# Kernel optimization log

Hardware: AMD Instinct MI355X
Metric: run time of the kernel (lower is better)

## Reference

```python
import jax, jax.numpy as jnp
import numpy as np

N = 50000      # nodes
E = 800000     # edges (avg degree 16)
D_IN, D_H, D_OUT = 128, 256, 128


def setup_inputs() -> dict:
    key = jax.random.key(0)
    ks = jax.random.split(key, 12)
    x = jax.random.normal(ks[0], (N, D_IN), jnp.float32)
    src = jax.random.randint(ks[1], (E,), 0, N)
    dst = jax.random.randint(ks[2], (E,), 0, N)

    def lin(k, din, dout):
        return (jax.random.normal(k, (din, dout), jnp.float32) / np.sqrt(din)).astype(jnp.float32)

    dims = [(D_IN, D_H), (D_H, D_H), (D_H, D_OUT)]
    params = {}
    ki = 3
    for i, (di, do) in enumerate(dims):
        params[f"W_self{i}"] = lin(ks[ki], di, do); ki += 1
        params[f"W_neigh{i}"] = lin(ks[ki], di, do); ki += 1
        params[f"b{i}"] = jnp.zeros((do,), jnp.float32)
    return {"x": x, "src": src, "dst": dst, **params}


def _mean_agg(h, src, dst):
    # gather src features along edges, segment-mean into dst nodes
    msg = jnp.take(h, src, axis=0)                              # [E, D]
    s = jax.ops.segment_sum(msg, dst, num_segments=N)           # [N, D]
    deg = jax.ops.segment_sum(jnp.ones((dst.shape[0], 1), h.dtype), dst, num_segments=N)
    return s / jnp.maximum(deg, 1.0)                            # zero-degree -> 0, as in DGL


def reference(x, src, dst,
              W_self0, W_neigh0, b0,
              W_self1, W_neigh1, b1,
              W_self2, W_neigh2, b2):
    Ws = [(W_self0, W_neigh0, b0), (W_self1, W_neigh1, b1), (W_self2, W_neigh2, b2)]
    h = x
    for i, (Ws_i, Wn_i, b_i) in enumerate(Ws):
        neigh = _mean_agg(h, src, dst)
        h = h @ Ws_i + neigh @ Wn_i + b_i                       # SAGEConv('mean')
        if i < len(Ws) - 1:
            h = jax.nn.relu(h)                                  # activation between layers
    return h
```

## Files before the change

### kernel.cpp

```cpp
#include <hip/hip_runtime.h>

#define NN 50000
#define NE 800000
#define NCHK 200
#define CHKE 4000
#define NBUK 196
#define BCAP 5120
#define NOFF (NBUK * NCHK)
#define NSB  ((NOFF + 255) / 256)

typedef __attribute__((ext_vector_type(8))) short short8;
typedef __attribute__((ext_vector_type(4))) float f32x4;
typedef unsigned int u32;
typedef unsigned short u16;

__device__ __forceinline__ float bf2f(short u) {
    union { unsigned int i; float f; } c;
    c.i = ((unsigned int)(unsigned short)u) << 16;
    return c.f;
}
__device__ __forceinline__ short f2bf(float f) {
    union { float f; unsigned int i; } c; c.f = f;
    unsigned int u = c.i;
    unsigned int r = (u + 0x7FFFu + ((u >> 16) & 1u)) >> 16;
    return (short)r;
}


__global__ void cvt_f32_bf16_kernel(const float* __restrict__ in, short* __restrict__ out, int n) {
    int gid = blockIdx.x * 256 + threadIdx.x;
    if (gid < n) out[gid] = f2bf(in[gid]);
}

__global__ void wcvt_all_kernel(const float* __restrict__ Ws0, const float* __restrict__ Wn0,
                                const float* __restrict__ Ws1, const float* __restrict__ Wn1,
                                const float* __restrict__ Ws2, const float* __restrict__ Wn2,
                                short* __restrict__ wts) {
    int gid = blockIdx.x * 256 + threadIdx.x;
    const float* W; int K, Dout, base, loc;
    if (gid < 65536)       { K = 128; Dout = 256; base = (gid < 32768)  ? 0 : 32768;
                             W = (gid < 32768)  ? Ws0 : Wn0; loc = gid & 32767; }
    else if (gid < 196608) { K = 256; Dout = 256; base = (gid < 131072) ? 65536 : 131072;
                             W = (gid < 131072) ? Ws1 : Wn1; loc = (gid - 65536) & 65535; }
    else                   { K = 256; Dout = 128; base = (gid < 229376) ? 196608 : 229376;
                             W = (gid < 229376) ? Ws2 : Wn2; loc = (gid - 196608) & 32767; }
    int k = loc / Dout, d = loc - k * Dout;
    int kt = k >> 6, kl = k & 63;
    wts[base + kt * Dout * 64 + d * 64 + (kl ^ ((d & 7) << 3))] = f2bf(W[(long)k * Dout + d]);
}

__global__ __launch_bounds__(256) void bucket_hist_kernel(const int* __restrict__ dst,
                                                          int* __restrict__ chist) {
    __shared__ int lh[NBUK];
    int b = blockIdx.x, t = threadIdx.x;
    for (int i = t; i < NBUK; i += 256) lh[i] = 0;
    __syncthreads();
    int base = b * CHKE;
    for (int i = t; i < CHKE; i += 256) atomicAdd(&lh[dst[base + i] >> 8], 1);
    __syncthreads();
    for (int i = t; i < NBUK; i += 256) chist[i * NCHK + b] = lh[i];
}

__global__ __launch_bounds__(256) void off_blocksum_kernel(const int* __restrict__ in,
                                                           int* __restrict__ bsum) {
    __shared__ int sm[256];
    int t = threadIdx.x;
    int idx = blockIdx.x * 256 + t;
    sm[t] = (idx < NOFF) ? in[idx] : 0;
    __syncthreads();
    for (int off = 128; off > 0; off >>= 1) {
        if (t < off) sm[t] += sm[t + off];
        __syncthreads();
    }
    if (t == 0) bsum[blockIdx.x] = sm[0];
}

__global__ __launch_bounds__(256) void off_scanb_kernel(const int* __restrict__ bsum,
                                                        int* __restrict__ bpre) {
    __shared__ int sm[256];
    int t = threadIdx.x;
    sm[t] = (t < NSB) ? bsum[t] : 0;
    __syncthreads();
    for (int o = 1; o < 256; o <<= 1) {
        int v = sm[t];
        int a = (t >= o) ? sm[t - o] : 0;
        __syncthreads();
        sm[t] = v + a;
        __syncthreads();
    }
    if (t < NSB) bpre[t] = (t == 0) ? 0 : sm[t - 1];
}

__global__ __launch_bounds__(256) void off_scatter_kernel(const int* __restrict__ in,
                                                          const int* __restrict__ bpre,
                                                          int* __restrict__ off) {
    __shared__ int sm[256];
    int t = threadIdx.x;
    int idx = blockIdx.x * 256 + t;
    int val = (idx < NOFF) ? in[idx] : 0;
    sm[t] = val;
    __syncthreads();
    for (int o = 1; o < 256; o <<= 1) {
        int v = sm[t];
        int a = (t >= o) ? sm[t - o] : 0;
        __syncthreads();
        sm[t] = v + a;
        __syncthreads();
    }
    if (idx < NOFF) off[idx] = bpre[blockIdx.x] + sm[t] - val;
}

__global__ __launch_bounds__(256) void bucket_scatter_kernel(const int* __restrict__ src,
                                                             const int* __restrict__ dst,
                                                             const int* __restrict__ off,
                                                             u32* __restrict__ ebuf) {
    __shared__ int lcur[NBUK];
    int b = blockIdx.x, t = threadIdx.x;
    for (int i = t; i < NBUK; i += 256) lcur[i] = off[i * NCHK + b];
    __syncthreads();
    int base = b * CHKE;
    for (int i = t; i < CHKE; i += 256) {
        int d = dst[base + i], s = src[base + i];
        int slot = atomicAdd(&lcur[d >> 8], 1);
        ebuf[slot] = ((u32)(d & 255) << 16) | (u32)s;
    }
}

__global__ __launch_bounds__(256) void bucket_sort_kernel(const u32* __restrict__ ebuf,
                                                          const int* __restrict__ off,
                                                          u16* __restrict__ srcs16,
                                                          int* __restrict__ row_start,
                                                          int* __restrict__ cnt) {
    __shared__ u32 earr[BCAP];
    __shared__ u16 s16[BCAP];
    __shared__ int lhist[256], lpre[256], lcur[256];
    int k = blockIdx.x, t = threadIdx.x;
    int base = off[k * NCHK];
    int end  = (k < NBUK - 1) ? off[(k + 1) * NCHK] : NE;
    int nE = end - base;
    lhist[t] = 0;
    __syncthreads();
    for (int i = t; i < nE; i += 256) {
        u32 e = ebuf[base + i];
        earr[i] = e;
        atomicAdd(&lhist[e >> 16], 1);
    }
    __syncthreads();
    int v = lhist[t];
    lpre[t] = v;
    __syncthreads();
    for (int o = 1; o < 256; o <<= 1) {
        int x = lpre[t];
        int a = (t >= o) ? lpre[t - o] : 0;
        __syncthreads();
        lpre[t] = x + a;
        __syncthreads();
    }
    int excl = lpre[t] - v;
    int node = k * 256 + t;
    if (node < NN) { row_start[node] = base + excl; cnt[node] = v; }
    lcur[t] = excl;
    __syncthreads();
    for (int i = t; i < nE; i += 256) {
        u32 e = earr[i];
        int pos = atomicAdd(&lcur[e >> 16], 1);
        s16[pos] = (u16)(e & 0xFFFFu);
    }
    __syncthreads();
    for (int i = t; i < nE; i += 256) srcs16[base + i] = s16[i];
}


template<int D>
__global__ __launch_bounds__(256) void gather_mean2_kernel(
    const short* __restrict__ h, const u16* __restrict__ srcs,
    const int* __restrict__ row_start, const int* __restrict__ cnt,
    short* __restrict__ nb)
{
    constexpr int CPR = D / 8;
    constexpr int EPL = 64 / CPR;
    const int wave = threadIdx.x >> 6;
    const int lane = threadIdx.x & 63;
    const int v = blockIdx.x * 4 + wave;
    if (v >= NN) return;
    const int c  = cnt[v];
    const int rs = row_start[v];
    const int slot = lane / CPR;
    const int cg   = lane & (CPR - 1);
    float acc[8];
    #pragma unroll
    for (int j = 0; j < 8; ++j) acc[j] = 0.f;
    const short8* hp = (const short8*)h;
    int i = slot;
    for (; i + 3 * EPL < c; i += 4 * EPL) {
        int s0 = srcs[rs + i];
        int s1 = srcs[rs + i + EPL];
        int s2 = srcs[rs + i + 2 * EPL];
        int s3 = srcs[rs + i + 3 * EPL];
        short8 v0 = hp[(size_t)s0 * CPR + cg];
        short8 v1 = hp[(size_t)s1 * CPR + cg];
        short8 v2 = hp[(size_t)s2 * CPR + cg];
        short8 v3 = hp[(size_t)s3 * CPR + cg];
        #pragma unroll
        for (int j = 0; j < 8; ++j)
            acc[j] += (bf2f(v0[j]) + bf2f(v1[j])) + (bf2f(v2[j]) + bf2f(v3[j]));
    }
    for (; i < c; i += EPL) {
        int s0 = srcs[rs + i];
        short8 v0 = hp[(size_t)s0 * CPR + cg];
        #pragma unroll
        for (int j = 0; j < 8; ++j) acc[j] += bf2f(v0[j]);
    }
    #pragma unroll
    for (int j = 0; j < 8; ++j) {
        if (EPL == 4) acc[j] += __shfl_xor(acc[j], 16);
        acc[j] += __shfl_xor(acc[j], 32);
    }
    if (slot == 0) {
        float inv = (c > 0) ? (1.0f / (float)c) : 0.0f;
        short8 outv;
        #pragma unroll
        for (int j = 0; j < 8; ++j) outv[j] = f2bf(acc[j] * inv);
        ((short8*)nb)[(size_t)v * CPR + cg] = outv;
    }
}

template<int NOUT, int KK, int PHASES, bool RELU, bool OUT_F32, bool ADDIN, bool BIAS>
__global__ __launch_bounds__(512, 2) void gemm_sage3_kernel(
    const short* __restrict__ Aself, const short* __restrict__ Aneigh,
    const short* __restrict__ Bself, const short* __restrict__ Bneigh,
    const float* __restrict__ bias, void* __restrict__ outp, int M,
    const short* __restrict__ addin)
{
    constexpr int WN = NOUT / 64;
    constexpr int WM = 8 / WN;
    constexpr int MR = 128 / (WM * 16);
    constexpr int NR = 4;
    constexpr int KT = KK / 64;
    constexpr int NT = PHASES * KT;
    constexpr int WC = NOUT / 64;

    __shared__ short ldsA[2][128 * 64];
    __shared__ short ldsW[2][NOUT * 64];

    const int tid  = threadIdx.x;
    const int wave = tid >> 6;
    const int lane = tid & 63;
    const int wm = wave / WN;
    const int wn = wave % WN;
    const int l15 = lane & 15;
    const int kg  = lane >> 4;
    const int bm  = blockIdx.x * 128;

    f32x4 acc[MR][NR];
    #pragma unroll
    for (int a = 0; a < MR; ++a)
        #pragma unroll
        for (int b = 0; b < NR; ++b)
            acc[a][b] = (f32x4){0.f, 0.f, 0.f, 0.f};

    const int srow = tid >> 3;
    const int scol = ((tid & 7) << 3) ^ ((srow & 7) << 3);

    auto stageA = [&](int buf, int t) {
        int ph = t / KT, kt = t - ph * KT;
        const short* A = ph ? Aneigh : Aself;
        #pragma unroll
        for (int c = 0; c < 2; ++c) {
            const short* gp = A + (size_t)(bm + c * 64 + srow) * KK + kt * 64 + scol;
            __builtin_amdgcn_global_load_lds(
                (const __attribute__((address_space(1))) u32*)gp,
                (__attribute__((address_space(3))) u32*)(&ldsA[buf][c * 4096 + (wave << 9)]),
                16, 0, 0);
        }
    };
    auto stageW = [&](int buf, int t) {
        int ph = t / KT, kt = t - ph * KT;
        const short* Wm = (ph ? Bneigh : Bself) + (size_t)kt * NOUT * 64 + tid * 8;
        #pragma unroll
        for (int c = 0; c < WC; ++c) {
            __builtin_amdgcn_global_load_lds(
                (const __attribute__((address_space(1))) u32*)(Wm + c * 4096),
                (__attribute__((address_space(3))) u32*)(&ldsW[buf][c * 4096 + (wave << 9)]),
                16, 0, 0);
        }
    };

    stageA(0, 0);
    stageW(0, 0);
    __syncthreads();

    for (int t = 0; t < NT; ++t) {
        const int cur = t & 1;
        if (t + 1 < NT) { stageA(cur ^ 1, t + 1); stageW(cur ^ 1, t + 1); }

        #pragma unroll
        for (int ks = 0; ks < 2; ++ks) {
            short8 areg[MR], wreg[NR];
            #pragma unroll
            for (int mr = 0; mr < MR; ++mr) {
                int r = wm * (MR * 16) + mr * 16 + l15;
                areg[mr] = *(const short8*)(&ldsA[cur][r * 64 + ((ks * 32 + kg * 8) ^ ((r & 7) << 3))]);
            }
            #pragma unroll
            for (int nr = 0; nr < NR; ++nr) {
                int cl = wn * 64 + nr * 16 + l15;
                wreg[nr] = *(const short8*)(&ldsW[cur][cl * 64 + ((ks * 32 + kg * 8) ^ ((cl & 7) << 3))]);
            }
            #pragma unroll
            for (int mr = 0; mr < MR; ++mr)
                #pragma unroll
                for (int nr = 0; nr < NR; ++nr)
                    acc[mr][nr] = __builtin_amdgcn_mfma_f32_16x16x32_bf16(
                        areg[mr], wreg[nr], acc[mr][nr], 0, 0, 0);
        }
        __syncthreads();
    }

    #pragma unroll
    for (int mr = 0; mr < MR; ++mr) {
        int rowb = bm + wm * (MR * 16) + mr * 16 + kg * 4;
        #pragma unroll
        for (int nr = 0; nr < NR; ++nr) {
            int col = wn * 64 + nr * 16 + l15;
            float bv = BIAS ? bias[col] : 0.f;
            #pragma unroll
            for (int r = 0; r < 4; ++r) {
                int row = rowb + r;
                if (row < M) {
                    float vv = acc[mr][nr][r] + bv;
                    if (ADDIN) vv += bf2f(addin[(size_t)row * NOUT + col]);
                    if (RELU) vv = fmaxf(vv, 0.f);
                    if (OUT_F32) ((float*)outp)[(size_t)row * NOUT + col] = vv;
                    else         ((short*)outp)[(size_t)row * NOUT + col] = f2bf(vv);
                }
            }
        }
    }
}


extern "C" void kernel_launch(void* const* d_in, const int* in_sizes, int n_in,
                              void* d_out, int out_size, void* d_ws, size_t ws_size,
                              hipStream_t stream) {
    const float* x    = (const float*)d_in[0];
    const int*   srcp = (const int*)d_in[1];
    const int*   dstp = (const int*)d_in[2];
    const float* Ws0  = (const float*)d_in[3];
    const float* Wn0  = (const float*)d_in[4];
    const float* b0   = (const float*)d_in[5];
    const float* Ws1  = (const float*)d_in[6];
    const float* Wn1  = (const float*)d_in[7];
    const float* b1   = (const float*)d_in[8];
    const float* Ws2  = (const float*)d_in[9];
    const float* Wn2  = (const float*)d_in[10];
    const float* b2   = (const float*)d_in[11];

    char* base = (char*)d_ws;
    size_t off_b = 0;
    auto alloc = [&](size_t bytes) -> void* {
        void* p = base + off_b;
        off_b += (bytes + 255) & ~(size_t)255;
        return p;
    };

    int*   cnt       = (int*)alloc((size_t)NN * 4);
    int*   row_start = (int*)alloc((size_t)NN * 4);
    int*   chist     = (int*)alloc((size_t)NOFF * 4);
    int*   offb      = (int*)alloc((size_t)NOFF * 4);
    int*   bsum      = (int*)alloc((size_t)NSB * 4);
    int*   bpre      = (int*)alloc((size_t)NSB * 4);
    u32*   ebuf      = (u32*)alloc((size_t)NE * 4);
    u16*   srcs16    = (u16*)alloc((size_t)NE * 2);
    short* hA        = (short*)alloc((size_t)NN * 256 * 2);
    short* hB        = (short*)alloc((size_t)NN * 256 * 2);
    short* nb        = (short*)alloc((size_t)NN * 256 * 2);
    short* wts       = (short*)alloc((size_t)262144 * 2 + 65536);
    short* Wt0s = wts;
    short* Wt0n = Wt0s + 32768;
    short* Wt1s = Wt0n + 32768;
    short* Wt1n = Wt1s + 65536;
    short* Wt2s = Wt1n + 65536;
    short* Wt2n = Wt2s + 32768;

    bucket_hist_kernel<<<NCHK, 256, 0, stream>>>(dstp, chist);
    off_blocksum_kernel<<<NSB, 256, 0, stream>>>(chist, bsum);
    off_scanb_kernel<<<1, 256, 0, stream>>>(bsum, bpre);
    off_scatter_kernel<<<NSB, 256, 0, stream>>>(chist, bpre, offb);
    bucket_scatter_kernel<<<NCHK, 256, 0, stream>>>(srcp, dstp, offb, ebuf);
    bucket_sort_kernel<<<NBUK, 256, 0, stream>>>(ebuf, offb, srcs16, row_start, cnt);

    wcvt_all_kernel<<<1024, 256, 0, stream>>>(Ws0, Wn0, Ws1, Wn1, Ws2, Wn2, wts);

    cvt_f32_bf16_kernel<<<(NN * 128 + 255) / 256, 256, 0, stream>>>(x, hA, NN * 128);

    const int mblocks = (NN + 127) / 128;
    const int gblocks = (NN + 3) / 4;

    gather_mean2_kernel<128><<<gblocks, 256, 0, stream>>>(hA, srcs16, row_start, cnt, nb);
    gemm_sage3_kernel<256, 128, 2, true, false, false, true><<<mblocks, 512, 0, stream>>>(
        hA, nb, Wt0s, Wt0n, b0, hB, NN, nullptr);

    gather_mean2_kernel<256><<<gblocks, 256, 0, stream>>>(hB, srcs16, row_start, cnt, nb);
    gemm_sage3_kernel<256, 256, 2, true, false, false, true><<<mblocks, 512, 0, stream>>>(
        hB, nb, Wt1s, Wt1n, b1, hA, NN, nullptr);

    gemm_sage3_kernel<128, 256, 1, false, false, false, false><<<mblocks, 512, 0, stream>>>(
        hA, hA, Wt2n, Wt2n, nullptr, hB, NN, nullptr);
    gather_mean2_kernel<128><<<gblocks, 256, 0, stream>>>(hB, srcs16, row_start, cnt, nb);
    gemm_sage3_kernel<128, 256, 1, false, true, true, true><<<mblocks, 512, 0, stream>>>(
        hA, hA, Wt2s, Wt2s, b2, d_out, NN, nb);
}
```

Baseline: 243.2 us.

## Load GEMM weights straight into registers in MFMA fragment order, drop LDS staging

The weight conversion kernel now writes each weight matrix in the exact per-lane MFMA fragment order. The GEMM kernel then loads a whole phase of weight fragments from global memory straight into registers, instead of double-buffering weight tiles through LDS. This removes the weight LDS buffers, the weight staging traffic and the LDS reads of weights from the inner loop. In exchange, each lane holds KT*2*NR short8 weight registers per phase alongside the accumulators, which risks register spills under the 512-thread, 2-blocks launch bound.

```diff
diff --git a/kernel.cpp b/kernel.cpp
--- a/kernel.cpp
+++ b/kernel.cpp
@@ -45,8 +45,10 @@
     else                   { K = 256; Dout = 128; base = (gid < 229376) ? 196608 : 229376;
                              W = (gid < 229376) ? Ws2 : Wn2; loc = (gid - 196608) & 32767; }
     int k = loc / Dout, d = loc - k * Dout;
-    int kt = k >> 6, kl = k & 63;
-    wts[base + kt * Dout * 64 + d * 64 + (kl ^ ((d & 7) << 3))] = f2bf(W[(long)k * Dout + d]);
+    int kt = k >> 6, ks = (k >> 5) & 1, kg = (k >> 3) & 3, j = k & 7;
+    int cgp = d >> 4, l = d & 15;
+    int off = ((((kt * 2 + ks) * (Dout >> 4) + cgp) * 4 + kg) * 16 + l) * 8 + j;
+    wts[base + off] = f2bf(W[(long)k * Dout + d]);
 }
 
 __global__ __launch_bounds__(256) void bucket_hist_kernel(const int* __restrict__ dst,
@@ -226,7 +228,7 @@
 }
 
 template<int NOUT, int KK, int PHASES, bool RELU, bool OUT_F32, bool ADDIN, bool BIAS>
-__global__ __launch_bounds__(512, 2) void gemm_sage3_kernel(
+__global__ __launch_bounds__(512, 2) void gemm_sage4_kernel(
     const short* __restrict__ Aself, const short* __restrict__ Aneigh,
     const short* __restrict__ Bself, const short* __restrict__ Bneigh,
     const float* __restrict__ bias, void* __restrict__ outp, int M,
@@ -238,10 +240,9 @@
     constexpr int NR = 4;
     constexpr int KT = KK / 64;
     constexpr int NT = PHASES * KT;
-    constexpr int WC = NOUT / 64;
+    constexpr int CG = NOUT / 16;
 
     __shared__ short ldsA[2][128 * 64];
-    __shared__ short ldsW[2][NOUT * 64];
 
     const int tid  = threadIdx.x;
     const int wave = tid >> 6;
@@ -274,47 +275,46 @@
                 16, 0, 0);
         }
     };
-    auto stageW = [&](int buf, int t) {
-        int ph = t / KT, kt = t - ph * KT;
-        const short* Wm = (ph ? Bneigh : Bself) + (size_t)kt * NOUT * 64 + tid * 8;
-        #pragma unroll
-        for (int c = 0; c < WC; ++c) {
-            __builtin_amdgcn_global_load_lds(
-                (const __attribute__((address_space(1))) u32*)(Wm + c * 4096),
-                (__attribute__((address_space(3))) u32*)(&ldsW[buf][c * 4096 + (wave << 9)]),
-                16, 0, 0);
-        }
-    };
 
     stageA(0, 0);
-    stageW(0, 0);
-    __syncthreads();
-
-    for (int t = 0; t < NT; ++t) {
-        const int cur = t & 1;
-        if (t + 1 < NT) { stageA(cur ^ 1, t + 1); stageW(cur ^ 1, t + 1); }
-
-        #pragma unroll
-        for (int ks = 0; ks < 2; ++ks) {
-            short8 areg[MR], wreg[NR];
+    __syncthreads();
+
+    #pragma unroll
+    for (int ph = 0; ph < PHASES; ++ph) {
+        const short* __restrict__ Wb = ph ? Bneigh : Bself;
+        short8 wreg[KT][2][NR];
+        #pragma unroll
+        for (int kt = 0; kt < KT; ++kt)
             #pragma unroll
-            for (int mr = 0; mr < MR; ++mr) {
-                int r = wm * (MR * 16) + mr * 16 + l15;
-                areg[mr] = *(const short8*)(&ldsA[cur][r * 64 + ((ks * 32 + kg * 8) ^ ((r & 7) << 3))]);
-            }
-            #pragma unroll
-            for (int nr = 0; nr < NR; ++nr) {
-                int cl = wn * 64 + nr * 16 + l15;
-                wreg[nr] = *(const short8*)(&ldsW[cur][cl * 64 + ((ks * 32 + kg * 8) ^ ((cl & 7) << 3))]);
-            }
-            #pragma unroll
-            for (int mr = 0; mr < MR; ++mr)
+            for (int ks = 0; ks < 2; ++ks)
                 #pragma unroll
                 for (int nr = 0; nr < NR; ++nr)
-                    acc[mr][nr] = __builtin_amdgcn_mfma_f32_16x16x32_bf16(
-                        areg[mr], wreg[nr], acc[mr][nr], 0, 0, 0);
+                    wreg[kt][ks][nr] = *(const short8*)(
+                        Wb + (size_t)((((kt * 2 + ks) * CG + wn * 4 + nr) * 4 + kg) * 16 + l15) * 8);
+
+        #pragma unroll
+        for (int kt = 0; kt < KT; ++kt) {
+            const int t = ph * KT + kt;
+            const int cur = t & 1;
+            if (t + 1 < NT) stageA(cur ^ 1, t + 1);
+
+            #pragma unroll
+            for (int ks = 0; ks < 2; ++ks) {
+                short8 areg[MR];
+                #pragma unroll
+                for (int mr = 0; mr < MR; ++mr) {
+                    int r = wm * (MR * 16) + mr * 16 + l15;
+                    areg[mr] = *(const short8*)(&ldsA[cur][r * 64 + ((ks * 32 + kg * 8) ^ ((r & 7) << 3))]);
+                }
+                #pragma unroll
+                for (int mr = 0; mr < MR; ++mr)
+                    #pragma unroll
+                    for (int nr = 0; nr < NR; ++nr)
+                        acc[mr][nr] = __builtin_amdgcn_mfma_f32_16x16x32_bf16(
+                            areg[mr], wreg[kt][ks][nr], acc[mr][nr], 0, 0, 0);
+            }
+            __syncthreads();
         }
-        __syncthreads();
     }
 
     #pragma unroll
@@ -398,16 +398,16 @@
     const int gblocks = (NN + 3) / 4;
 
     gather_mean2_kernel<128><<<gblocks, 256, 0, stream>>>(hA, srcs16, row_start, cnt, nb);
-    gemm_sage3_kernel<256, 128, 2, true, false, false, true><<<mblocks, 512, 0, stream>>>(
+    gemm_sage4_kernel<256, 128, 2, true, false, false, true><<<mblocks, 512, 0, stream>>>(
         hA, nb, Wt0s, Wt0n, b0, hB, NN, nullptr);
 
     gather_mean2_kernel<256><<<gblocks, 256, 0, stream>>>(hB, srcs16, row_start, cnt, nb);
-    gemm_sage3_kernel<256, 256, 2, true, false, false, true><<<mblocks, 512, 0, stream>>>(
+    gemm_sage4_kernel<256, 256, 2, true, false, false, true><<<mblocks, 512, 0, stream>>>(
         hB, nb, Wt1s, Wt1n, b1, hA, NN, nullptr);
 
-    gemm_sage3_kernel<128, 256, 1, false, false, false, false><<<mblocks, 512, 0, stream>>>(
+    gemm_sage4_kernel<128, 256, 1, false, false, false, false><<<mblocks, 512, 0, stream>>>(
         hA, hA, Wt2n, Wt2n, nullptr, hB, NN, nullptr);
     gather_mean2_kernel<128><<<gblocks, 256, 0, stream>>>(hB, srcs16, row_start, cnt, nb);
-    gemm_sage3_kernel<128, 256, 1, false, true, true, true><<<mblocks, 512, 0, stream>>>(
+    gemm_sage4_kernel<128, 256, 1, false, true, true, true><<<mblocks, 512, 0, stream>>>(
         hA, hA, Wt2s, Wt2s, b2, d_out, NN, nb);
 }
```

After: 246.8 us. Within noise of the previous version (+1.5%).
